# Kernel tuning notes

Measured on AMD Instinct MI355X. Metric: run time of the kernel, lower is better.

The kernel has to match this reference:

```python
import jax, jax.numpy as jnp
import numpy as np

N = 8192; E = 262144
CS = 384; CZ = 128; CH = 16; H = 12; PQK = 4; PV = 8
INF = 1e5; EPS = 1e-8
S_QK = float(1.0 / np.sqrt(3.0 * CH))        # sqrt(1/(3*c_hidden))
S_B = float(1.0 / np.sqrt(3.0))              # sqrt(1/3)
S_PT = float(1.0 / np.sqrt(3.0 * (PQK * 9.0 / 2.0)))


def setup_inputs() -> dict:
    key = jax.random.key(0)
    ks = jax.random.split(key, 16)
    def w(k, shape, fan_in):
        return jax.random.normal(k, shape, jnp.float32) * (1.0 / float(np.sqrt(fan_in)))
    d = {}
    d["s"] = jax.random.normal(ks[0], (N, CS), jnp.float32)
    d["z"] = jax.random.normal(ks[1], (E, CZ), jnp.float32)
    d["edge_index"] = jax.random.randint(ks[2], (2, E), 0, N, jnp.int32)
    d["rot"] = jax.random.normal(ks[3], (N, 3, 3), jnp.float32)
    d["trans"] = jax.random.normal(ks[4], (N, 3), jnp.float32)
    d["mask"] = jnp.ones((N,), jnp.float32)
    d["q_w"] = w(ks[5], (CS, H * CH), CS);              d["q_b"] = jnp.zeros((H * CH,), jnp.float32)
    d["kv_w"] = w(ks[6], (CS, 2 * H * CH), CS);         d["kv_b"] = jnp.zeros((2 * H * CH,), jnp.float32)
    d["qp_w"] = w(ks[7], (CS, H * PQK * 3), CS);        d["qp_b"] = jnp.zeros((H * PQK * 3,), jnp.float32)
    d["kvp_w"] = w(ks[8], (CS, H * (PQK + PV) * 3), CS); d["kvp_b"] = jnp.zeros((H * (PQK + PV) * 3,), jnp.float32)
    d["b_w"] = w(ks[9], (CZ, H), CZ);                   d["b_b"] = jnp.zeros((H,), jnp.float32)
    d["dz_w"] = w(ks[10], (CZ, CZ // 4), CZ);           d["dz_b"] = jnp.zeros((CZ // 4,), jnp.float32)
    d["head_weights"] = jnp.full((H,), float(np.log(np.e - 1.0)), jnp.float32)
    cdim = H * (CZ // 4 + CH + PV * 4)
    d["out_w"] = w(ks[11], (cdim, CS), cdim);           d["out_b"] = jnp.zeros((CS,), jnp.float32)
    return d


def reference(s, z, edge_index, rot, trans, mask,
              q_w, q_b, kv_w, kv_b, qp_w, qp_b, kvp_w, kvp_b,
              b_w, b_b, dz_w, dz_b, head_weights, out_w, out_b):
    src = edge_index[1]
    dst = edge_index[0]

    def to_pts(y, P):
        # y: [N, H*P*3] -> split into (x,y,z) chunks -> [N, H*P, 3], then rigid-apply
        xyz = jnp.stack(jnp.split(y, 3, axis=-1), axis=-1)          # [N, H*P, 3]
        pts = jnp.einsum('nij,npj->npi', rot, xyz) + trans[:, None, :]
        return pts.reshape(N, H, P, 3)

    q = (s @ q_w + q_b).reshape(N, H, CH)
    kv = (s @ kv_w + kv_b).reshape(N, H, 2 * CH)
    k, v = kv[..., :CH], kv[..., CH:]

    q_pts = to_pts(s @ qp_w + qp_b, PQK)                            # [N,H,PQK,3]
    kv_pts = to_pts(s @ kvp_w + kvp_b, PQK + PV)                    # [N,H,PQK+PV,3]
    k_pts, v_pts = kv_pts[..., :PQK, :], kv_pts[..., PQK:, :]

    b = z @ b_w + b_b                                               # [E, H]

    # scalar attention logits
    a = jnp.einsum('ehc,ehc->eh', q[src], k[dst]) * S_QK + S_B * b  # [E, H]

    # point attention logits
    disp = q_pts[src] - k_pts[dst]                                  # [E,H,PQK,3]
    pt_att = jnp.sum(disp * disp, axis=-1)                          # [E,H,PQK]
    hw = jax.nn.softplus(head_weights) * S_PT                       # [H]
    pt_att = -0.5 * jnp.sum(pt_att * hw[None, :, None], axis=-1)    # [E,H]

    edge_mask = INF * (mask[dst] * mask[src] - 1.0)                 # [E]
    a = a + pt_att + edge_mask[:, None]

    # scatter softmax over src segments (pyg-style)
    amax = jax.ops.segment_max(a, src, num_segments=N)
    amax = jnp.where(jnp.isfinite(amax), amax, 0.0)
    ex = jnp.exp(a - amax[src])
    denom = jax.ops.segment_sum(ex, src, num_segments=N)
    a = ex / (denom[src] + 1e-16)                                   # [E,H]

    # weighted scatter-reduce aggregations
    o = jax.ops.segment_sum(a[..., None] * v[dst], src, num_segments=N).reshape(N, H * CH)
    o_pt = jax.ops.segment_sum(a[..., None, None] * v_pts[dst], src, num_segments=N)  # [N,H,PV,3]
    # invert_apply: R^T (p - t)
    o_pt = jnp.einsum('nji,nhpj->nhpi', rot, o_pt - trans[:, None, None, :])
    o_pt_norm = jnp.sqrt(jnp.sum(o_pt * o_pt, axis=-1) + EPS).reshape(N, H * PV)
    o_pt_flat = o_pt.reshape(N, H * PV, 3)

    pair_z = z @ dz_w + dz_b                                        # [E, CZ//4]
    o_pair = jax.ops.segment_sum(a[..., None] * pair_z[:, None, :], src, num_segments=N).reshape(N, H * (CZ // 4))

    feats = jnp.concatenate(
        [o, o_pt_flat[..., 0], o_pt_flat[..., 1], o_pt_flat[..., 2], o_pt_norm, o_pair], axis=-1)
    return feats @ out_w + out_b
```

## Files before the change

### kernel.cpp

```cpp
#include <hip/hip_runtime.h>
#include <math.h>

#define NN 8192
#define EE 262144
#define CSD 384
#define CZD 128
#define HH 12
#define MAXDEG 96
#define ABLD 13

#define S_QK 0.14433756729740643f
#define S_B  0.5773502691896258f
#define S_PT 0.1360827634879543f

typedef __bf16 bf16;
typedef __attribute__((ext_vector_type(8))) __bf16 bf16x8;
typedef __attribute__((ext_vector_type(4))) __bf16 bf16x4;
typedef __attribute__((ext_vector_type(4))) float floatx4;

#define OFF_LIN    0
#define OFF_QPACK  (OFF_LIN + NN*1152)
#define OFF_KPACK  (OFF_QPACK + NN*336)
#define OFF_VPACK  (OFF_KPACK + NN*336)
#define OFF_BZ     (OFF_VPACK + NN*480)
#define OFF_SBF    (OFF_BZ + EE*44)
#define OFF_WCAT   (OFF_SBF + NN*192)
#define OFF_OWT    (OFF_WCAT + 221184)
#define OFF_FEATB  (OFF_OWT + 184320)
#define OFF_BZW    (OFF_FEATB + NN*480)
#define OFF_BZB    (OFF_BZW + 3072)
#define OFF_BIASC  (OFF_BZB + 48)
#define OFF_INTS   (OFF_BIASC + 1152)

__global__ void count_kernel(const int* __restrict__ ei, int* __restrict__ counts) {
    int e = blockIdx.x * 256 + threadIdx.x;
    if (e < EE) atomicAdd(&counts[ei[EE + e]], 1);
}

__global__ __launch_bounds__(1024) void scan_kernel(const int* __restrict__ counts,
                                                    int* __restrict__ offs,
                                                    int* __restrict__ cursor) {
    __shared__ int part[1024];
    int t = threadIdx.x;
    int local[8];
    int s = 0;
    #pragma unroll
    for (int j = 0; j < 8; ++j) { local[j] = counts[t * 8 + j]; s += local[j]; }
    part[t] = s;
    __syncthreads();
    for (int off = 1; off < 1024; off <<= 1) {
        int vv = 0;
        if (t >= off) vv = part[t - off];
        __syncthreads();
        if (t >= off) part[t] += vv;
        __syncthreads();
    }
    int run = (t == 0) ? 0 : part[t - 1];
    #pragma unroll
    for (int j = 0; j < 8; ++j) {
        offs[t * 8 + j] = run;
        cursor[t * 8 + j] = run;
        run += local[j];
    }
    if (t == 1023) offs[NN] = run;
}

__global__ void fill_kernel(const int* __restrict__ ei, int* __restrict__ cursor,
                            int* __restrict__ elist) {
    int e = blockIdx.x * 256 + threadIdx.x;
    if (e < EE) {
        int s = ei[EE + e];
        int pos = atomicAdd(&cursor[s], 1);
        elist[pos] = e;
    }
}

__global__ void cvt_s_kernel(const float* __restrict__ s, bf16* __restrict__ sbf) {
    int i = blockIdx.x * 256 + threadIdx.x;
    float4 v = *(const float4*)(s + (long)i * 4);
    bf16x4 o = {(__bf16)v.x, (__bf16)v.y, (__bf16)v.z, (__bf16)v.w};
    *(bf16x4*)(sbf + (long)i * 4) = o;
}

__global__ void build_wcat(const float* __restrict__ q_w, const float* __restrict__ kv_w,
                           const float* __restrict__ qp_w, const float* __restrict__ kvp_w,
                           const float* __restrict__ q_b, const float* __restrict__ kv_b,
                           const float* __restrict__ qp_b, const float* __restrict__ kvp_b,
                           bf16* __restrict__ wt, float* __restrict__ bias_cat) {
    int id = blockIdx.x * 256 + threadIdx.x;
    if (id >= 1152 * 384) return;
    int n = id / 384, k = id - n * 384;
    float v;
    if (n < 192)      v = q_w[k * 192 + n];
    else if (n < 576) v = kv_w[k * 384 + (n - 192)];
    else if (n < 720) v = qp_w[k * 144 + (n - 576)];
    else              v = kvp_w[k * 432 + (n - 720)];
    wt[id] = (__bf16)v;
    if (k == 0) {
        float b;
        if (n < 192)      b = q_b[n];
        else if (n < 576) b = kv_b[n - 192];
        else if (n < 720) b = qp_b[n - 576];
        else              b = kvp_b[n - 720];
        bias_cat[n] = b;
    }
}

__global__ void build_owt(const float* __restrict__ out_w, bf16* __restrict__ wt) {
    int id = blockIdx.x * 256 + threadIdx.x;
    if (id >= 384 * 960) return;
    int n = id / 960, k = id - n * 960;
    wt[id] = (__bf16)out_w[k * 384 + n];
}

__global__ void build_bzw(const float* __restrict__ b_w, const float* __restrict__ b_b,
                          const float* __restrict__ dz_w, const float* __restrict__ dz_b,
                          bf16* __restrict__ wt, float* __restrict__ bias) {
    int id = blockIdx.x * 256 + threadIdx.x;
    if (id < 48 * 128) {
        int c = id / 128, k = id - c * 128;
        float v = 0.f;
        if (c < 12)      v = b_w[k * 12 + c];
        else if (c < 44) v = dz_w[k * 32 + (c - 12)];
        wt[id] = (__bf16)v;
    }
    if (id < 44) bias[id] = (id < 12) ? b_b[id] : dz_b[id - 12];
}

#define LDKP 40
__global__ __launch_bounds__(256) void gemm_mfma_bt(const bf16* __restrict__ A,
                                                    const bf16* __restrict__ BT,
                                                    const float* __restrict__ bias,
                                                    float* __restrict__ C,
                                                    int M, int K, int N) {
    __shared__ __align__(16) bf16 As[128][LDKP];
    __shared__ __align__(16) bf16 Bs[128][LDKP];
    const int tid = threadIdx.x;
    const int bm = blockIdx.y * 128;
    const int bn = blockIdx.x * 128;
    const int wave = tid >> 6, lane = tid & 63;
    const int wr = (wave >> 1) * 64;
    const int wc = (wave & 1) * 64;
    const int lm = lane & 15;
    const int kg = lane >> 4;

    floatx4 acc[4][4];
    #pragma unroll
    for (int i = 0; i < 4; ++i)
        #pragma unroll
        for (int j = 0; j < 4; ++j) acc[i][j] = (floatx4){0.f, 0.f, 0.f, 0.f};

    const int srow = tid >> 2;
    const int skoff = (tid & 3) * 8;

    for (int k0 = 0; k0 < K; k0 += 32) {
        __syncthreads();
        *(float4*)(&As[srow][skoff])      = *(const float4*)(A + (long)(bm + srow) * K + k0 + skoff);
        *(float4*)(&As[srow + 64][skoff]) = *(const float4*)(A + (long)(bm + srow + 64) * K + k0 + skoff);
        *(float4*)(&Bs[srow][skoff])      = *(const float4*)(BT + (long)(bn + srow) * K + k0 + skoff);
        *(float4*)(&Bs[srow + 64][skoff]) = *(const float4*)(BT + (long)(bn + srow + 64) * K + k0 + skoff);
        __syncthreads();
        bf16x8 af[4], bfr[4];
        #pragma unroll
        for (int i = 0; i < 4; ++i) af[i] = *(const bf16x8*)(&As[wr + i * 16 + lm][kg * 8]);
        #pragma unroll
        for (int j = 0; j < 4; ++j) bfr[j] = *(const bf16x8*)(&Bs[wc + j * 16 + lm][kg * 8]);
        #pragma unroll
        for (int i = 0; i < 4; ++i)
            #pragma unroll
            for (int j = 0; j < 4; ++j)
                acc[i][j] = __builtin_amdgcn_mfma_f32_16x16x32_bf16(af[i], bfr[j], acc[i][j], 0, 0, 0);
    }

    const int crow0 = bm + wr + kg * 4;
    const int ccol0 = bn + wc + lm;
    #pragma unroll
    for (int i = 0; i < 4; ++i) {
        #pragma unroll
        for (int j = 0; j < 4; ++j) {
            int col = ccol0 + j * 16;
            float b = bias[col];
            #pragma unroll
            for (int r = 0; r < 4; ++r)
                C[(long)(crow0 + i * 16 + r) * N + col] = acc[i][j][r] + b;
        }
    }
}

#define BZLD 136
__global__ __launch_bounds__(256) void gemm_bz(const float* __restrict__ z,
                                               const bf16* __restrict__ BT,
                                               const float* __restrict__ bias,
                                               float* __restrict__ bz) {
    __shared__ __align__(16) bf16 As[128][BZLD];
    __shared__ __align__(16) bf16 Bs[48][BZLD];
    const int tid = threadIdx.x;
    const int bm = blockIdx.x * 128;
    {
        int row = tid >> 1, half = tid & 1;
        const float* zr = z + (long)(bm + row) * 128 + half * 64;
        #pragma unroll
        for (int j = 0; j < 8; ++j) {
            float4 a0 = *(const float4*)(zr + j * 8);
            float4 a1 = *(const float4*)(zr + j * 8 + 4);
            bf16x8 o = {(__bf16)a0.x, (__bf16)a0.y, (__bf16)a0.z, (__bf16)a0.w,
                        (__bf16)a1.x, (__bf16)a1.y, (__bf16)a1.z, (__bf16)a1.w};
            *(bf16x8*)(&As[row][half * 64 + j * 8]) = o;
        }
    }
    for (int idx = tid; idx < 48 * 16; idx += 256) {
        int r = idx >> 4, seg = idx & 15;
        *(bf16x8*)(&Bs[r][seg * 8]) = *(const bf16x8*)(BT + r * 128 + seg * 8);
    }
    __syncthreads();
    const int wave = tid >> 6, lane = tid & 63;
    const int lm = lane & 15, kg = lane >> 4;
    const int rowbase = wave * 32;
    floatx4 acc[2][3];
    #pragma unroll
    for (int i = 0; i < 2; ++i)
        #pragma unroll
        for (int j = 0; j < 3; ++j) acc[i][j] = (floatx4){0.f, 0.f, 0.f, 0.f};
    #pragma unroll
    for (int ks = 0; ks < 4; ++ks) {
        bf16x8 af[2], bfr[3];
        #pragma unroll
        for (int i = 0; i < 2; ++i) af[i] = *(const bf16x8*)(&As[rowbase + i * 16 + lm][ks * 32 + kg * 8]);
        #pragma unroll
        for (int j = 0; j < 3; ++j) bfr[j] = *(const bf16x8*)(&Bs[j * 16 + lm][ks * 32 + kg * 8]);
        #pragma unroll
        for (int i = 0; i < 2; ++i)
            #pragma unroll
            for (int j = 0; j < 3; ++j)
                acc[i][j] = __builtin_amdgcn_mfma_f32_16x16x32_bf16(af[i], bfr[j], acc[i][j], 0, 0, 0);
    }
    #pragma unroll
    for (int i = 0; i < 2; ++i) {
        int r0 = bm + rowbase + i * 16 + kg * 4;
        #pragma unroll
        for (int j = 0; j < 3; ++j) {
            int col = j * 16 + lm;
            if (col < 44) {
                float b = bias[col];
                #pragma unroll
                for (int r = 0; r < 4; ++r)
                    bz[(long)(r0 + r) * 44 + col] = acc[i][j][r] + b;
            }
        }
    }
}

__global__ void pack_kernel(const float* __restrict__ lin,
                            const float* __restrict__ rot, const float* __restrict__ trans,
                            float* __restrict__ qpack, float* __restrict__ kpack,
                            float* __restrict__ vpack) {
    int n = blockIdx.x;
    int t = threadIdx.x;
    const float* row = lin + (long)n * 1152;
    const float* R = rot + n * 9;
    float tx = trans[n * 3 + 0], ty = trans[n * 3 + 1], tz = trans[n * 3 + 2];
    {
        int h = t >> 4, c = t & 15;
        qpack[(long)n * 336 + h * 28 + c] = row[h * 16 + c];
        kpack[(long)n * 336 + h * 28 + c] = row[192 + h * 32 + c];
        vpack[(long)n * 480 + h * 40 + c] = row[192 + h * 32 + 16 + c];
    }
    float x, y, z;
    if (t < 48) {
        x = row[576 + t]; y = row[624 + t]; z = row[672 + t];
    } else {
        int u = t - 48;
        x = row[720 + u]; y = row[864 + u]; z = row[1008 + u];
    }
    float ox = R[0] * x + R[1] * y + R[2] * z + tx;
    float oy = R[3] * x + R[4] * y + R[5] * z + ty;
    float oz = R[6] * x + R[7] * y + R[8] * z + tz;
    if (t < 48) {
        int h = t >> 2, p = t & 3;
        long b = (long)n * 336 + h * 28 + 16 + p * 3;
        qpack[b] = ox; qpack[b + 1] = oy; qpack[b + 2] = oz;
    } else {
        int u = t - 48;
        int h = u / 12, j = u - h * 12;
        if (j < 4) {
            long b = (long)n * 336 + h * 28 + 16 + j * 3;
            kpack[b] = ox; kpack[b + 1] = oy; kpack[b + 2] = oz;
        } else {
            long b = (long)n * 480 + h * 40 + 16 + (j - 4) * 3;
            vpack[b] = ox; vpack[b + 1] = oy; vpack[b + 2] = oz;
        }
    }
}

__global__ __launch_bounds__(256) void agg_fused(const int* __restrict__ offs,
                                                 const int* __restrict__ elist,
                                                 const int* __restrict__ ei,
                                                 const float* __restrict__ qpack,
                                                 const float* __restrict__ kpack,
                                                 const float* __restrict__ vpack,
                                                 const float* __restrict__ bz,
                                                 const float* __restrict__ mask,
                                                 const float* __restrict__ head_w,
                                                 const float* __restrict__ rot,
                                                 const float* __restrict__ trans,
                                                 bf16* __restrict__ feats) {
    const int wave = threadIdx.x >> 6;
    const int lane = threadIdx.x & 63;
    const int n = blockIdx.x * 4 + wave;

    __shared__ float abuf_all[4][MAXDEG * ABLD];
    __shared__ float q_all[4][352];
    __shared__ int   emeta_all[4][MAXDEG];
    __shared__ int   dmeta_all[4][MAXDEG];
    __shared__ float mmeta_all[4][MAXDEG];
    float* abuf = abuf_all[wave];
    float* q_s  = q_all[wave];
    int*   emeta = emeta_all[wave];
    int*   dmeta = dmeta_all[wave];
    float* mmeta = mmeta_all[wave];

    const int beg = offs[n];
    int deg = offs[n + 1] - beg;
    if (deg > MAXDEG) deg = MAXDEG;

    for (int idx = lane; idx < 84; idx += 64)
        *(float4*)(&q_s[idx * 4]) = *(const float4*)(qpack + (long)n * 336 + idx * 4);
    if (lane < 12) q_s[336 + lane] = log1pf(expf(head_w[lane])) * S_PT;
    const float msrc = mask[n];

    if (lane < deg) {
        int e = elist[beg + lane];
        int d = ei[e];
        emeta[lane] = e; dmeta[lane] = d; mmeta[lane] = mask[d];
    }
    if (64 + lane < deg) {
        int e = elist[beg + 64 + lane];
        int d = ei[e];
        emeta[64 + lane] = e; dmeta[64 + lane] = d; mmeta[64 + lane] = mask[d];
    }
    __syncthreads();

    for (int idx = lane; idx < deg * 12; idx += 64) {
        int c = idx / 12, h = idx - c * 12;
        int e = emeta[c];
        int d = dmeta[c];
        float md = mmeta[c];
        const float* kh = kpack + (long)d * 336 + h * 28;
        const float* qh = &q_s[h * 28];
        float qk = 0.f;
        #pragma unroll
        for (int i = 0; i < 16; ++i) qk += qh[i] * kh[i];
        float pt = 0.f;
        #pragma unroll
        for (int i = 0; i < 12; ++i) {
            float d2 = qh[16 + i] - kh[16 + i];
            pt += d2 * d2;
        }
        float b = bz[(long)e * 44 + h];
        abuf[c * ABLD + h] = qk * S_QK + S_B * b - 0.5f * q_s[336 + h] * pt
                           + 100000.0f * (msrc * md - 1.0f);
    }
    __syncthreads();

    {
        float lg0[12], lg1[12];
        const bool a0 = lane < deg, a1 = 64 + lane < deg;
        #pragma unroll
        for (int h = 0; h < 12; ++h) {
            lg0[h] = a0 ? abuf[lane * ABLD + h] : -1e30f;
            lg1[h] = a1 ? abuf[(64 + lane) * ABLD + h] : -1e30f;
        }
        #pragma unroll
        for (int h = 0; h < 12; ++h) {
            float mx = fmaxf(lg0[h], lg1[h]);
            #pragma unroll
            for (int off = 32; off > 0; off >>= 1) mx = fmaxf(mx, __shfl_xor(mx, off));
            if (!isfinite(mx)) mx = 0.f;
            float w0 = a0 ? __expf(lg0[h] - mx) : 0.f;
            float w1 = a1 ? __expf(lg1[h] - mx) : 0.f;
            float sm = w0 + w1;
            #pragma unroll
            for (int off = 32; off > 0; off >>= 1) sm += __shfl_xor(sm, off);
            float rl = 1.f / (sm + 1e-16f);
            if (a0) abuf[lane * ABLD + h] = w0 * rl;
            if (a1) abuf[(64 + lane) * ABLD + h] = w1 * rl;
        }
    }
    __syncthreads();

    int hh[4], off4[4];
    bool pr[4], act[4];
    #pragma unroll
    for (int r = 0; r < 4; ++r) {
        int slot = r * 64 + lane;
        act[r] = slot < 216;
        if (slot < 120) {
            hh[r] = slot / 10;
            off4[r] = (slot - hh[r] * 10) * 4 + hh[r] * 40;
            pr[r] = false;
        } else if (slot < 216) {
            int u = slot - 120;
            hh[r] = u >> 3;
            off4[r] = 12 + (u & 7) * 4;
            pr[r] = true;
        } else {
            hh[r] = 0; off4[r] = 0; pr[r] = false;
        }
    }
    floatx4 acc[4];
    #pragma unroll
    for (int r = 0; r < 4; ++r) acc[r] = (floatx4){0.f, 0.f, 0.f, 0.f};

    #pragma unroll 2
    for (int c = 0; c < deg; ++c) {
        int eC = emeta[c];
        int dC = dmeta[c];
        const float* vpb = vpack + (long)dC * 480;
        const float* bpb = bz + (long)eC * 44;
        #pragma unroll
        for (int r = 0; r < 4; ++r) {
            float w = abuf[c * ABLD + hh[r]];
            const float* srcp = pr[r] ? bpb : vpb;
            floatx4 v = *(const floatx4*)(srcp + off4[r]);
            acc[r] += w * v;
        }
    }
    __syncthreads();

    float* opt_s = q_s;
    #pragma unroll
    for (int r = 0; r < 4; ++r) {
        if (!act[r]) continue;
        int slot = r * 64 + lane;
        if (slot < 120) {
            int h = hh[r], q4 = slot - h * 10;
            if (q4 < 4) {
                bf16x4 o = {(__bf16)acc[r][0], (__bf16)acc[r][1], (__bf16)acc[r][2], (__bf16)acc[r][3]};
                *(bf16x4*)(feats + (long)n * 960 + h * 16 + q4 * 4) = o;
            } else {
                *(floatx4*)(&opt_s[h * 24 + (q4 - 4) * 4]) = acc[r];
            }
        } else {
            int u = slot - 120, h = u >> 3, seg = u & 7;
            bf16x4 o = {(__bf16)acc[r][0], (__bf16)acc[r][1], (__bf16)acc[r][2], (__bf16)acc[r][3]};
            *(bf16x4*)(feats + (long)n * 960 + 576 + h * 32 + seg * 4) = o;
        }
    }
    __syncthreads();

    const float* R = rot + n * 9;
    float tx = trans[n * 3 + 0], ty = trans[n * 3 + 1], tz = trans[n * 3 + 2];
    for (int idx = lane; idx < 96; idx += 64) {
        int h = idx >> 3, p = idx & 7;
        float x = opt_s[h * 24 + p * 3 + 0] - tx;
        float y = opt_s[h * 24 + p * 3 + 1] - ty;
        float zc = opt_s[h * 24 + p * 3 + 2] - tz;
        float ox = R[0] * x + R[3] * y + R[6] * zc;
        float oy = R[1] * x + R[4] * y + R[7] * zc;
        float oz = R[2] * x + R[5] * y + R[8] * zc;
        float nrm = sqrtf(ox * ox + oy * oy + oz * oz + 1e-8f);
        feats[(long)n * 960 + 192 + idx] = (__bf16)ox;
        feats[(long)n * 960 + 288 + idx] = (__bf16)oy;
        feats[(long)n * 960 + 384 + idx] = (__bf16)oz;
        feats[(long)n * 960 + 480 + idx] = (__bf16)nrm;
    }
}

extern "C" void kernel_launch(void* const* d_in, const int* in_sizes, int n_in,
                              void* d_out, int out_size, void* d_ws, size_t ws_size,
                              hipStream_t stream) {
    const float* s      = (const float*)d_in[0];
    const float* z      = (const float*)d_in[1];
    const int*   ei     = (const int*)d_in[2];
    const float* rot    = (const float*)d_in[3];
    const float* trans  = (const float*)d_in[4];
    const float* mask   = (const float*)d_in[5];
    const float* q_w    = (const float*)d_in[6];
    const float* q_b    = (const float*)d_in[7];
    const float* kv_w   = (const float*)d_in[8];
    const float* kv_b   = (const float*)d_in[9];
    const float* qp_w   = (const float*)d_in[10];
    const float* qp_b   = (const float*)d_in[11];
    const float* kvp_w  = (const float*)d_in[12];
    const float* kvp_b  = (const float*)d_in[13];
    const float* b_w    = (const float*)d_in[14];
    const float* b_b    = (const float*)d_in[15];
    const float* dz_w   = (const float*)d_in[16];
    const float* dz_b   = (const float*)d_in[17];
    const float* head_w = (const float*)d_in[18];
    const float* out_w  = (const float*)d_in[19];
    const float* out_b  = (const float*)d_in[20];

    float* ws      = (float*)d_ws;
    float* lin     = ws + OFF_LIN;
    float* qpack   = ws + OFF_QPACK;
    float* kpack   = ws + OFF_KPACK;
    float* vpack   = ws + OFF_VPACK;
    float* bz      = ws + OFF_BZ;
    bf16*  sbf     = (bf16*)(ws + OFF_SBF);
    bf16*  wcat    = (bf16*)(ws + OFF_WCAT);
    bf16*  owt     = (bf16*)(ws + OFF_OWT);
    bf16*  featb   = (bf16*)(ws + OFF_FEATB);
    bf16*  bzwbf   = (bf16*)(ws + OFF_BZW);
    float* bzb     = ws + OFF_BZB;
    float* biasc   = ws + OFF_BIASC;
    int* ints   = (int*)(ws + OFF_INTS);
    int* offs   = ints;
    int* cursor = ints + NN + 1;
    int* counts = ints + 2 * NN + 1;
    int* elist  = ints + 3 * NN + 1;

    hipMemsetAsync(counts, 0, NN * sizeof(int), stream);
    count_kernel<<<EE / 256, 256, 0, stream>>>(ei, counts);
    scan_kernel<<<1, 1024, 0, stream>>>(counts, offs, cursor);
    fill_kernel<<<EE / 256, 256, 0, stream>>>(ei, cursor, elist);

    cvt_s_kernel<<<NN * CSD / 4 / 256, 256, 0, stream>>>(s, sbf);
    build_wcat<<<(1152 * 384 + 255) / 256, 256, 0, stream>>>(q_w, kv_w, qp_w, kvp_w,
                                                             q_b, kv_b, qp_b, kvp_b, wcat, biasc);
    build_owt<<<(384 * 960 + 255) / 256, 256, 0, stream>>>(out_w, owt);
    build_bzw<<<(48 * 128 + 255) / 256, 256, 0, stream>>>(b_w, b_b, dz_w, dz_b, bzwbf, bzb);

    gemm_mfma_bt<<<dim3(1152 / 128, NN / 128), 256, 0, stream>>>(sbf, wcat, biasc, lin, NN, CSD, 1152);

    pack_kernel<<<NN, 192, 0, stream>>>(lin, rot, trans, qpack, kpack, vpack);

    gemm_bz<<<EE / 128, 256, 0, stream>>>(z, bzwbf, bzb, bz);

    agg_fused<<<NN / 4, 256, 0, stream>>>(offs, elist, ei, qpack, kpack, vpack, bz,
                                          mask, head_w, rot, trans, featb);

    gemm_mfma_bt<<<dim3(384 / 128, NN / 128), 256, 0, stream>>>(featb, owt, out_b, (float*)d_out, NN, 960, 384);
}
```

Baseline: 501.7 us.

## Store gathered K/V/pair features in bf16 and schedule nodes by degree

The key, value and pair-embedding tensors gathered per edge in the aggregation kernel are now stored in bf16 with padded, 16-byte aligned layouts, so they can be read with wide vector loads. This halves the bytes fetched in the gather-bound loop. A new single-block counting sort orders nodes by descending degree so waves in a block have similar work. The edge bias logits stay fp32, and the bf16 rounding of points and values adds some numerical error.

```diff
diff --git a/kernel.cpp b/kernel.cpp
--- a/kernel.cpp
+++ b/kernel.cpp
@@ -20,10 +20,11 @@
 
 #define OFF_LIN    0
 #define OFF_QPACK  (OFF_LIN + NN*1152)
-#define OFF_KPACK  (OFF_QPACK + NN*336)
-#define OFF_VPACK  (OFF_KPACK + NN*336)
-#define OFF_BZ     (OFF_VPACK + NN*480)
-#define OFF_SBF    (OFF_BZ + EE*44)
+#define OFF_KPACKH (OFF_QPACK + NN*336)
+#define OFF_VPACKH (OFF_KPACKH + NN*192)
+#define OFF_BLOG   (OFF_VPACKH + NN*240)
+#define OFF_PAIRH  (OFF_BLOG + EE*12)
+#define OFF_SBF    (OFF_PAIRH + EE*16)
 #define OFF_WCAT   (OFF_SBF + NN*192)
 #define OFF_OWT    (OFF_WCAT + 221184)
 #define OFF_FEATB  (OFF_OWT + 184320)
@@ -72,6 +73,32 @@
         int s = ei[EE + e];
         int pos = atomicAdd(&cursor[s], 1);
         elist[pos] = e;
+    }
+}
+
+__global__ __launch_bounds__(1024) void sort_kernel(const int* __restrict__ offs,
+                                                    int* __restrict__ order) {
+    __shared__ int hist[256];
+    __shared__ int base[256];
+    int t = threadIdx.x;
+    if (t < 256) hist[t] = 0;
+    __syncthreads();
+    for (int n = t; n < NN; n += 1024) {
+        int d = offs[n + 1] - offs[n];
+        if (d > 255) d = 255;
+        atomicAdd(&hist[d], 1);
+    }
+    __syncthreads();
+    if (t == 0) {
+        int run = 0;
+        for (int d = 255; d >= 0; --d) { base[d] = run; run += hist[d]; }
+    }
+    __syncthreads();
+    for (int n = t; n < NN; n += 1024) {
+        int d = offs[n + 1] - offs[n];
+        if (d > 255) d = 255;
+        int pos = atomicAdd(&base[d], 1);
+        order[pos] = n;
     }
 }
 
@@ -191,7 +218,8 @@
 __global__ __launch_bounds__(256) void gemm_bz(const float* __restrict__ z,
                                                const bf16* __restrict__ BT,
                                                const float* __restrict__ bias,
-                                               float* __restrict__ bz) {
+                                               float* __restrict__ blog,
+                                               bf16* __restrict__ pairh) {
     __shared__ __align__(16) bf16 As[128][BZLD];
     __shared__ __align__(16) bf16 Bs[48][BZLD];
     const int tid = threadIdx.x;
@@ -240,11 +268,16 @@
         #pragma unroll
         for (int j = 0; j < 3; ++j) {
             int col = j * 16 + lm;
-            if (col < 44) {
+            if (col < 12) {
                 float b = bias[col];
                 #pragma unroll
                 for (int r = 0; r < 4; ++r)
-                    bz[(long)(r0 + r) * 44 + col] = acc[i][j][r] + b;
+                    blog[(long)(r0 + r) * 12 + col] = acc[i][j][r] + b;
+            } else if (col < 44) {
+                float b = bias[col];
+                #pragma unroll
+                for (int r = 0; r < 4; ++r)
+                    pairh[(long)(r0 + r) * 32 + (col - 12)] = (__bf16)(acc[i][j][r] + b);
             }
         }
     }
@@ -252,8 +285,8 @@
 
 __global__ void pack_kernel(const float* __restrict__ lin,
                             const float* __restrict__ rot, const float* __restrict__ trans,
-                            float* __restrict__ qpack, float* __restrict__ kpack,
-                            float* __restrict__ vpack) {
+                            float* __restrict__ qpack, bf16* __restrict__ kpackh,
+                            bf16* __restrict__ vpackh) {
     int n = blockIdx.x;
     int t = threadIdx.x;
     const float* row = lin + (long)n * 1152;
@@ -262,8 +295,13 @@
     {
         int h = t >> 4, c = t & 15;
         qpack[(long)n * 336 + h * 28 + c] = row[h * 16 + c];
-        kpack[(long)n * 336 + h * 28 + c] = row[192 + h * 32 + c];
-        vpack[(long)n * 480 + h * 40 + c] = row[192 + h * 32 + 16 + c];
+        kpackh[(long)n * 384 + h * 32 + c] = (__bf16)row[192 + h * 32 + c];
+        vpackh[(long)n * 480 + h * 40 + c] = (__bf16)row[192 + h * 32 + 16 + c];
+    }
+    if (t < 48 && (t & 3) == 0) {
+        int h = t >> 2;
+        #pragma unroll
+        for (int j = 0; j < 4; ++j) kpackh[(long)n * 384 + h * 32 + 28 + j] = (__bf16)0.f;
     }
     float x, y, z;
     if (t < 48) {
@@ -283,11 +321,11 @@
         int u = t - 48;
         int h = u / 12, j = u - h * 12;
         if (j < 4) {
-            long b = (long)n * 336 + h * 28 + 16 + j * 3;
-            kpack[b] = ox; kpack[b + 1] = oy; kpack[b + 2] = oz;
+            long b = (long)n * 384 + h * 32 + 16 + j * 3;
+            kpackh[b] = (__bf16)ox; kpackh[b + 1] = (__bf16)oy; kpackh[b + 2] = (__bf16)oz;
         } else {
             long b = (long)n * 480 + h * 40 + 16 + (j - 4) * 3;
-            vpack[b] = ox; vpack[b + 1] = oy; vpack[b + 2] = oz;
+            vpackh[b] = (__bf16)ox; vpackh[b + 1] = (__bf16)oy; vpackh[b + 2] = (__bf16)oz;
         }
     }
 }
@@ -295,10 +333,12 @@
 __global__ __launch_bounds__(256) void agg_fused(const int* __restrict__ offs,
                                                  const int* __restrict__ elist,
                                                  const int* __restrict__ ei,
+                                                 const int* __restrict__ order,
                                                  const float* __restrict__ qpack,
-                                                 const float* __restrict__ kpack,
-                                                 const float* __restrict__ vpack,
-                                                 const float* __restrict__ bz,
+                                                 const bf16* __restrict__ kpackh,
+                                                 const bf16* __restrict__ vpackh,
+                                                 const float* __restrict__ blog,
+                                                 const bf16* __restrict__ pairh,
                                                  const float* __restrict__ mask,
                                                  const float* __restrict__ head_w,
                                                  const float* __restrict__ rot,
@@ -306,15 +346,15 @@
                                                  bf16* __restrict__ feats) {
     const int wave = threadIdx.x >> 6;
     const int lane = threadIdx.x & 63;
-    const int n = blockIdx.x * 4 + wave;
+    const int n = order[blockIdx.x * 4 + wave];
 
     __shared__ float abuf_all[4][MAXDEG * ABLD];
-    __shared__ float q_all[4][352];
+    __shared__ __align__(16) float q_all[4][352];
     __shared__ int   emeta_all[4][MAXDEG];
     __shared__ int   dmeta_all[4][MAXDEG];
     __shared__ float mmeta_all[4][MAXDEG];
-    float* abuf = abuf_all[wave];
-    float* q_s  = q_all[wave];
+    float* abuf  = abuf_all[wave];
+    float* q_s   = q_all[wave];
     int*   emeta = emeta_all[wave];
     int*   dmeta = dmeta_all[wave];
     float* mmeta = mmeta_all[wave];
@@ -345,18 +385,22 @@
         int e = emeta[c];
         int d = dmeta[c];
         float md = mmeta[c];
-        const float* kh = kpack + (long)d * 336 + h * 28;
+        const bf16* khp = kpackh + (long)d * 384 + h * 32;
+        bf16x8 k0 = *(const bf16x8*)khp;
+        bf16x8 k1 = *(const bf16x8*)(khp + 8);
+        bf16x8 p0 = *(const bf16x8*)(khp + 16);
+        bf16x8 p1 = *(const bf16x8*)(khp + 24);
         const float* qh = &q_s[h * 28];
-        float qk = 0.f;
-        #pragma unroll
-        for (int i = 0; i < 16; ++i) qk += qh[i] * kh[i];
-        float pt = 0.f;
-        #pragma unroll
-        for (int i = 0; i < 12; ++i) {
-            float d2 = qh[16 + i] - kh[16 + i];
-            pt += d2 * d2;
-        }
-        float b = bz[(long)e * 44 + h];
+        float qk = 0.f, pt = 0.f;
+        #pragma unroll
+        for (int i = 0; i < 8; ++i) qk += qh[i] * (float)k0[i];
+        #pragma unroll
+        for (int i = 0; i < 8; ++i) qk += qh[8 + i] * (float)k1[i];
+        #pragma unroll
+        for (int i = 0; i < 8; ++i) { float dd = qh[16 + i] - (float)p0[i]; pt += dd * dd; }
+        #pragma unroll
+        for (int i = 0; i < 4; ++i) { float dd = qh[24 + i] - (float)p1[i]; pt += dd * dd; }
+        float b = blog[(long)e * 12 + h];
         abuf[c * ABLD + h] = qk * S_QK + S_B * b - 0.5f * q_s[336 + h] * pt
                            + 100000.0f * (msrc * md - 1.0f);
     }
@@ -388,62 +432,72 @@
     }
     __syncthreads();
 
-    int hh[4], off4[4];
-    bool pr[4], act[4];
-    #pragma unroll
-    for (int r = 0; r < 4; ++r) {
+    int hh[2], off8[2];
+    bool pr[2], act[2];
+    #pragma unroll
+    for (int r = 0; r < 2; ++r) {
         int slot = r * 64 + lane;
-        act[r] = slot < 216;
-        if (slot < 120) {
-            hh[r] = slot / 10;
-            off4[r] = (slot - hh[r] * 10) * 4 + hh[r] * 40;
-            pr[r] = false;
-        } else if (slot < 216) {
-            int u = slot - 120;
-            hh[r] = u >> 3;
-            off4[r] = 12 + (u & 7) * 4;
-            pr[r] = true;
+        if (slot < 60) {
+            hh[r] = slot / 5;
+            off8[r] = hh[r] * 40 + (slot - hh[r] * 5) * 8;
+            pr[r] = false; act[r] = true;
+        } else if (slot < 108) {
+            int u2 = slot - 60;
+            hh[r] = u2 >> 2;
+            off8[r] = (u2 & 3) * 8;
+            pr[r] = true; act[r] = true;
         } else {
-            hh[r] = 0; off4[r] = 0; pr[r] = false;
-        }
-    }
-    floatx4 acc[4];
-    #pragma unroll
-    for (int r = 0; r < 4; ++r) acc[r] = (floatx4){0.f, 0.f, 0.f, 0.f};
+            hh[r] = 0; off8[r] = 0; pr[r] = false; act[r] = false;
+        }
+    }
+    float acc[2][8];
+    #pragma unroll
+    for (int r = 0; r < 2; ++r)
+        #pragma unroll
+        for (int i = 0; i < 8; ++i) acc[r][i] = 0.f;
 
     #pragma unroll 2
     for (int c = 0; c < deg; ++c) {
         int eC = emeta[c];
         int dC = dmeta[c];
-        const float* vpb = vpack + (long)dC * 480;
-        const float* bpb = bz + (long)eC * 44;
-        #pragma unroll
-        for (int r = 0; r < 4; ++r) {
-            float w = abuf[c * ABLD + hh[r]];
-            const float* srcp = pr[r] ? bpb : vpb;
-            floatx4 v = *(const floatx4*)(srcp + off4[r]);
-            acc[r] += w * v;
-        }
-    }
-    __syncthreads();
+        const bf16* vpb = vpackh + (long)dC * 480;
+        const bf16* ppb = pairh + (long)eC * 32;
+        #pragma unroll
+        for (int r = 0; r < 2; ++r) {
+            if (act[r]) {
+                float w = abuf[c * ABLD + hh[r]];
+                bf16x8 v = *(const bf16x8*)((pr[r] ? ppb : vpb) + off8[r]);
+                #pragma unroll
+                for (int i = 0; i < 8; ++i) acc[r][i] += w * (float)v[i];
+            }
+        }
+    }
 
     float* opt_s = q_s;
     #pragma unroll
-    for (int r = 0; r < 4; ++r) {
+    for (int r = 0; r < 2; ++r) {
         if (!act[r]) continue;
         int slot = r * 64 + lane;
-        if (slot < 120) {
-            int h = hh[r], q4 = slot - h * 10;
-            if (q4 < 4) {
-                bf16x4 o = {(__bf16)acc[r][0], (__bf16)acc[r][1], (__bf16)acc[r][2], (__bf16)acc[r][3]};
-                *(bf16x4*)(feats + (long)n * 960 + h * 16 + q4 * 4) = o;
+        if (!pr[r]) {
+            int h = hh[r], u = slot - h * 5;
+            if (u < 2) {
+                bf16* fp = feats + (long)n * 960 + h * 16 + u * 8;
+                bf16x4 o1 = {(__bf16)acc[r][0], (__bf16)acc[r][1], (__bf16)acc[r][2], (__bf16)acc[r][3]};
+                bf16x4 o2 = {(__bf16)acc[r][4], (__bf16)acc[r][5], (__bf16)acc[r][6], (__bf16)acc[r][7]};
+                *(bf16x4*)fp = o1;
+                *(bf16x4*)(fp + 4) = o2;
             } else {
-                *(floatx4*)(&opt_s[h * 24 + (q4 - 4) * 4]) = acc[r];
+                float* op = &opt_s[h * 24 + (u - 2) * 8];
+                *(floatx4*)op = (floatx4){acc[r][0], acc[r][1], acc[r][2], acc[r][3]};
+                *(floatx4*)(op + 4) = (floatx4){acc[r][4], acc[r][5], acc[r][6], acc[r][7]};
             }
         } else {
-            int u = slot - 120, h = u >> 3, seg = u & 7;
-            bf16x4 o = {(__bf16)acc[r][0], (__bf16)acc[r][1], (__bf16)acc[r][2], (__bf16)acc[r][3]};
-            *(bf16x4*)(feats + (long)n * 960 + 576 + h * 32 + seg * 4) = o;
+            int u2 = slot - 60, h = u2 >> 2, seg = u2 & 3;
+            bf16* fp = feats + (long)n * 960 + 576 + h * 32 + seg * 8;
+            bf16x4 o1 = {(__bf16)acc[r][0], (__bf16)acc[r][1], (__bf16)acc[r][2], (__bf16)acc[r][3]};
+            bf16x4 o2 = {(__bf16)acc[r][4], (__bf16)acc[r][5], (__bf16)acc[r][6], (__bf16)acc[r][7]};
+            *(bf16x4*)fp = o1;
+            *(bf16x4*)(fp + 4) = o2;
         }
     }
     __syncthreads();
@@ -494,9 +548,10 @@
     float* ws      = (float*)d_ws;
     float* lin     = ws + OFF_LIN;
     float* qpack   = ws + OFF_QPACK;
-    float* kpack   = ws + OFF_KPACK;
-    float* vpack   = ws + OFF_VPACK;
-    float* bz      = ws + OFF_BZ;
+    bf16*  kpackh  = (bf16*)(ws + OFF_KPACKH);
+    bf16*  vpackh  = (bf16*)(ws + OFF_VPACKH);
+    float* blog    = ws + OFF_BLOG;
+    bf16*  pairh   = (bf16*)(ws + OFF_PAIRH);
     bf16*  sbf     = (bf16*)(ws + OFF_SBF);
     bf16*  wcat    = (bf16*)(ws + OFF_WCAT);
     bf16*  owt     = (bf16*)(ws + OFF_OWT);
@@ -509,11 +564,13 @@
     int* cursor = ints + NN + 1;
     int* counts = ints + 2 * NN + 1;
     int* elist  = ints + 3 * NN + 1;
+    int* order  = ints + 3 * NN + 1 + EE;
 
     hipMemsetAsync(counts, 0, NN * sizeof(int), stream);
     count_kernel<<<EE / 256, 256, 0, stream>>>(ei, counts);
     scan_kernel<<<1, 1024, 0, stream>>>(counts, offs, cursor);
     fill_kernel<<<EE / 256, 256, 0, stream>>>(ei, cursor, elist);
+    sort_kernel<<<1, 1024, 0, stream>>>(offs, order);
 
     cvt_s_kernel<<<NN * CSD / 4 / 256, 256, 0, stream>>>(s, sbf);
     build_wcat<<<(1152 * 384 + 255) / 256, 256, 0, stream>>>(q_w, kv_w, qp_w, kvp_w,
@@ -523,12 +580,12 @@
 
     gemm_mfma_bt<<<dim3(1152 / 128, NN / 128), 256, 0, stream>>>(sbf, wcat, biasc, lin, NN, CSD, 1152);
 
-    pack_kernel<<<NN, 192, 0, stream>>>(lin, rot, trans, qpack, kpack, vpack);
-
-    gemm_bz<<<EE / 128, 256, 0, stream>>>(z, bzwbf, bzb, bz);
-
-    agg_fused<<<NN / 4, 256, 0, stream>>>(offs, elist, ei, qpack, kpack, vpack, bz,
-                                          mask, head_w, rot, trans, featb);
+    pack_kernel<<<NN, 192, 0, stream>>>(lin, rot, trans, qpack, kpackh, vpackh);
+
+    gemm_bz<<<EE / 128, 256, 0, stream>>>(z, bzwbf, bzb, blog, pairh);
+
+    agg_fused<<<NN / 4, 256, 0, stream>>>(offs, elist, ei, order, qpack, kpackh, vpackh,
+                                          blog, pairh, mask, head_w, rot, trans, featb);
 
     gemm_mfma_bt<<<dim3(384 / 128, NN / 128), 256, 0, stream>>>(featb, owt, out_b, (float*)d_out, NN, 960, 384);
 }
```

Measured after the change: 461.6 us. -8.0%, faster.
